# Kernel tuning notes

Measured on AMD Instinct MI355X. Metric: run time of the kernel, lower is better.

The kernel has to match this reference:

```python
import jax, jax.numpy as jnp
import numpy as np

L, B, D = 2048, 8, 2048


def setup_inputs() -> dict:
    key = jax.random.key(0)
    k1, k2, k3 = jax.random.split(key, 3)
    x = jax.random.normal(k1, (L, B, D), dtype=jnp.float32)
    x_mix_last = jnp.zeros((B, D), dtype=jnp.float32)
    factor_param = jax.random.uniform(k2, (D,), dtype=jnp.float32)
    W = jax.random.normal(k3, (D, D), dtype=jnp.float32) * (1.0 / np.sqrt(D))
    return {"x": x, "x_mix_last": x_mix_last, "factor_param": factor_param, "W": W}


def reference(x, x_mix_last, factor_param, W):
    seq_len = x.shape[0]
    factor = jax.nn.sigmoid(factor_param)                      # [D]
    t = jnp.arange(seq_len, dtype=x.dtype)[:, None]            # [L,1]
    factor_progression = jnp.power(factor[None, :], t)         # [L,D] = factor**t
    # FFT-based causal convolution: y[t] = sum_{s<=t} factor**(t-s) * x[s]
    n = 2 * seq_len
    fft_fp = jnp.fft.rfft(factor_progression, n=n, axis=0)     # [L+1, D]
    fft_x = jnp.fft.rfft(x, n=n, axis=0)                       # [L+1, B, D]
    conv = jnp.fft.irfft(fft_x * fft_fp[:, None, :], axis=0)[:seq_len]  # [L,B,D]
    conv = conv.astype(x.dtype)
    # EMA mix: carried state decays as factor**(t+1); new input weighted by (1-factor)
    x_mix = (x_mix_last[None, :, :] * factor_progression[:, None, :] * factor
             + (1.0 - factor) * conv)                          # [L,B,D]
    # Linear mixing W (no bias): out = x_mix @ W.T
    return jnp.einsum('lbd,ed->lbe', x_mix, W)
```

## Files before the change

kernel.cpp:

```cpp
#include <hip/hip_runtime.h>
#include <hip/hip_bf16.h>
#include <stdint.h>

#define L_SEQ 2048
#define BATCH 8
#define DIM   2048
#define M_DIM (L_SEQ * BATCH)
#define N_DIM DIM
#define K_DIM DIM

typedef short bf16x8 __attribute__((ext_vector_type(8)));
typedef float f32x4  __attribute__((ext_vector_type(4)));
typedef unsigned short u16x4 __attribute__((ext_vector_type(4)));

__device__ inline unsigned short f2bf_rn(float f) {
    unsigned int u = __float_as_uint(f);
    u += 0x7FFF + ((u >> 16) & 1);
    return (unsigned short)(u >> 16);
}

__device__ inline void gload16(const void* g, void* l) {
    __builtin_amdgcn_global_load_lds(
        (const __attribute__((address_space(1))) void*)g,
        (__attribute__((address_space(3))) void*)l, 16, 0, 0);
}

__global__ void cvt_w_kernel(const float* __restrict__ W,
                             unsigned short* __restrict__ Wb) {
    int i = blockIdx.x * 256 + threadIdx.x;
    const float4 v = *reinterpret_cast<const float4*>(W + (size_t)i * 4);
    u16x4 r;
    r.x = f2bf_rn(v.x); r.y = f2bf_rn(v.y);
    r.z = f2bf_rn(v.z); r.w = f2bf_rn(v.w);
    *reinterpret_cast<u16x4*>(Wb + (size_t)i * 4) = r;
}

#define SCAN_CHUNK 256
#define SCAN_LB    128
__global__ void ema_scan_kernel(const float* __restrict__ x,
                                const float* __restrict__ xml,
                                const float* __restrict__ fparam,
                                unsigned short* __restrict__ xm) {
    int g  = blockIdx.x * 256 + threadIdx.x;
    int d  = g & (DIM - 1);
    int b  = (g >> 11) & (BATCH - 1);
    int ch = g >> 14;

    const float p  = fparam[d];
    const float f  = 1.0f / (1.0f + expf(-p));
    const float xl = xml[b * DIM + d];
    const float omf = 1.0f - f;

    const int t0 = ch * SCAN_CHUNK;
    int tstart = t0 - SCAN_LB; if (tstart < 0) tstart = 0;
    const int stride = BATCH * DIM;

    const float* xp = x + (size_t)tstart * stride + b * DIM + d;
    float conv = 0.0f;
    #pragma unroll 4
    for (int t = tstart; t < t0; ++t) {
        conv = fmaf(conv, f, *xp);
        xp += stride;
    }
    float pw = powf(f, (float)(t0 + 1));
    unsigned short* op = xm + (size_t)t0 * stride + b * DIM + d;
    #pragma unroll 4
    for (int t = 0; t < SCAN_CHUNK; ++t) {
        conv = fmaf(conv, f, *xp);
        float r = fmaf(xl, pw, omf * conv);
        *op = f2bf_rn(r);
        pw *= f;
        xp += stride; op += stride;
    }
}

#define BM 128
#define BN 128
#define BK 32

__global__ void gemm_bt_kernel(const unsigned short* __restrict__ A,
                               const unsigned short* __restrict__ Bt,
                               float* __restrict__ C) {
    __shared__ unsigned short lds_a[2][BM * BK];
    __shared__ unsigned short lds_b[2][BN * BK];

    int bid = blockIdx.x;
    int swz = (bid & 7) * 256 + (bid >> 3);
    int tm = swz >> 4;
    int tn = swz & 15;

    const int tid  = threadIdx.x;
    const int lane = tid & 63;
    const int w    = tid >> 6;
    const int wm   = (w >> 1) * 64;
    const int wn   = (w & 1) * 64;

    const int c0 = tid, c1 = tid + 256;
    const char* gA = (const char*)(A  + (size_t)tm * BM * K_DIM);
    const char* gB = (const char*)(Bt + (size_t)tn * BN * K_DIM);
    const char* pa0 = gA + (size_t)(c0 >> 2) * (K_DIM * 2) + (c0 & 3) * 16;
    const char* pa1 = gA + (size_t)(c1 >> 2) * (K_DIM * 2) + (c1 & 3) * 16;
    const char* pb0 = gB + (size_t)(c0 >> 2) * (K_DIM * 2) + (c0 & 3) * 16;
    const char* pb1 = gB + (size_t)(c1 >> 2) * (K_DIM * 2) + (c1 & 3) * 16;

#define STAGE(buf, t) do {                                   \
        size_t ko = (size_t)(t) * (BK * 2);                  \
        gload16(pa0 + ko, &lds_a[buf][c0 * 8]);              \
        gload16(pa1 + ko, &lds_a[buf][c1 * 8]);              \
        gload16(pb0 + ko, &lds_b[buf][c0 * 8]);              \
        gload16(pb1 + ko, &lds_b[buf][c1 * 8]);              \
    } while (0)

    f32x4 acc[4][4];
    #pragma unroll
    for (int m = 0; m < 4; ++m)
        #pragma unroll
        for (int n = 0; n < 4; ++n)
            acc[m][n] = (f32x4){0.f, 0.f, 0.f, 0.f};

    STAGE(0, 0);
    __syncthreads();

    const int rsel = lane & 15;
    const int kb   = (lane >> 4) * 8;

    int cur = 0;
    const int NT = K_DIM / BK;
    for (int t = 0; t < NT; ++t) {
        if (t + 1 < NT) STAGE(cur ^ 1, t + 1);

        bf16x8 afr[4], bfr[4];
        #pragma unroll
        for (int m = 0; m < 4; ++m)
            afr[m] = *(const bf16x8*)&lds_a[cur][(wm + m * 16 + rsel) * BK + kb];
        #pragma unroll
        for (int n = 0; n < 4; ++n)
            bfr[n] = *(const bf16x8*)&lds_b[cur][(wn + n * 16 + rsel) * BK + kb];

        #pragma unroll
        for (int m = 0; m < 4; ++m)
            #pragma unroll
            for (int n = 0; n < 4; ++n)
                acc[m][n] = __builtin_amdgcn_mfma_f32_16x16x32_bf16(
                    afr[m], bfr[n], acc[m][n], 0, 0, 0);

        __syncthreads();
        cur ^= 1;
    }

    float* Cp = C + (size_t)(tm * BM + wm) * N_DIM + tn * BN + wn;
    const int col = lane & 15;
    const int rg  = (lane >> 4) * 4;
    #pragma unroll
    for (int m = 0; m < 4; ++m)
        #pragma unroll
        for (int n = 0; n < 4; ++n)
            #pragma unroll
            for (int j = 0; j < 4; ++j)
                Cp[(size_t)(m * 16 + rg + j) * N_DIM + n * 16 + col] = acc[m][n][j];
#undef STAGE
}

extern "C" void kernel_launch(void* const* d_in, const int* in_sizes, int n_in,
                              void* d_out, int out_size, void* d_ws, size_t ws_size,
                              hipStream_t stream) {
    const float* x   = (const float*)d_in[0];
    const float* xml = (const float*)d_in[1];
    const float* fp  = (const float*)d_in[2];
    const float* W   = (const float*)d_in[3];
    float* out = (float*)d_out;

    unsigned short* xmix = (unsigned short*)d_ws;
    unsigned short* wb   = xmix + (size_t)M_DIM * K_DIM;

    cvt_w_kernel<<<4096, 256, 0, stream>>>(W, wb);
    ema_scan_kernel<<<512, 256, 0, stream>>>(x, xml, fp, xmix);
    gemm_bt_kernel<<<(M_DIM / BM) * (N_DIM / BN), 256, 0, stream>>>(xmix, wb, out);
}
```

Before: 449.3 us.

## Replace GEMM with 256x256 swizzled-LDS pipelined kernel and vectorize EMA scan

Replaces the 128x128 bf16 GEMM with a 256x256 tile, 512-thread kernel using 64-wide K tiles, XOR-swizzled LDS, and an eight-phase interleaved prefetch/MFMA schedule with explicit waitcnt and priority hints. The aim is higher operand reuse and better overlap of global loads with matrix math. The EMA scan now processes two channels per thread with float2 loads and uses shorter chunks and lookback for more parallelism. The GEMM uses 128KB of dynamic LDS, which limits occupancy, and the hand-tuned wait counts must match the load order exactly.

```diff
diff --git a/kernel.cpp b/kernel.cpp
--- a/kernel.cpp
+++ b/kernel.cpp
@@ -35,130 +35,180 @@
     *reinterpret_cast<u16x4*>(Wb + (size_t)i * 4) = r;
 }
 
-#define SCAN_CHUNK 256
-#define SCAN_LB    128
+#define SCH 128
+#define SLB 64
 __global__ void ema_scan_kernel(const float* __restrict__ x,
                                 const float* __restrict__ xml,
                                 const float* __restrict__ fparam,
                                 unsigned short* __restrict__ xm) {
     int g  = blockIdx.x * 256 + threadIdx.x;
-    int d  = g & (DIM - 1);
-    int b  = (g >> 11) & (BATCH - 1);
-    int ch = g >> 14;
-
-    const float p  = fparam[d];
-    const float f  = 1.0f / (1.0f + expf(-p));
-    const float xl = xml[b * DIM + d];
-    const float omf = 1.0f - f;
-
-    const int t0 = ch * SCAN_CHUNK;
-    int tstart = t0 - SCAN_LB; if (tstart < 0) tstart = 0;
-    const int stride = BATCH * DIM;
-
-    const float* xp = x + (size_t)tstart * stride + b * DIM + d;
-    float conv = 0.0f;
-    #pragma unroll 4
-    for (int t = tstart; t < t0; ++t) {
-        conv = fmaf(conv, f, *xp);
-        xp += stride;
+    int dp = (g & 1023) * 2;
+    int b  = (g >> 10) & (BATCH - 1);
+    int ch = g >> 13;
+
+    float2 pv = *reinterpret_cast<const float2*>(fparam + dp);
+    const float f0 = 1.0f / (1.0f + expf(-pv.x));
+    const float f1 = 1.0f / (1.0f + expf(-pv.y));
+    float2 xlv = *reinterpret_cast<const float2*>(xml + b * DIM + dp);
+    const float om0 = 1.0f - f0, om1 = 1.0f - f1;
+
+    const int t0 = ch * SCH;
+    int ts = t0 - SLB; if (ts < 0) ts = 0;
+    const int stride2 = (BATCH * DIM) / 2;
+
+    const float2* xp = reinterpret_cast<const float2*>(x) +
+                       (size_t)ts * stride2 + (b * DIM + dp) / 2;
+    float c0 = 0.0f, c1 = 0.0f;
+    #pragma unroll 8
+    for (int t = ts; t < t0; ++t) {
+        float2 v = *xp;
+        c0 = fmaf(c0, f0, v.x);
+        c1 = fmaf(c1, f1, v.y);
+        xp += stride2;
     }
-    float pw = powf(f, (float)(t0 + 1));
-    unsigned short* op = xm + (size_t)t0 * stride + b * DIM + d;
-    #pragma unroll 4
-    for (int t = 0; t < SCAN_CHUNK; ++t) {
-        conv = fmaf(conv, f, *xp);
-        float r = fmaf(xl, pw, omf * conv);
-        *op = f2bf_rn(r);
-        pw *= f;
-        xp += stride; op += stride;
+    float pw0 = powf(f0, (float)(t0 + 1));
+    float pw1 = powf(f1, (float)(t0 + 1));
+    ushort2* op = reinterpret_cast<ushort2*>(xm + (size_t)t0 * BATCH * DIM + b * DIM + dp);
+    #pragma unroll 8
+    for (int k = 0; k < SCH; ++k) {
+        float2 v = *xp;
+        c0 = fmaf(c0, f0, v.x);
+        c1 = fmaf(c1, f1, v.y);
+        ushort2 r;
+        r.x = f2bf_rn(fmaf(xlv.x, pw0, om0 * c0));
+        r.y = f2bf_rn(fmaf(xlv.y, pw1, om1 * c1));
+        *op = r;
+        pw0 *= f0; pw1 *= f1;
+        xp += stride2; op += stride2;
     }
 }
 
-#define BM 128
-#define BN 128
-#define BK 32
-
-__global__ void gemm_bt_kernel(const unsigned short* __restrict__ A,
-                               const unsigned short* __restrict__ Bt,
-                               float* __restrict__ C) {
-    __shared__ unsigned short lds_a[2][BM * BK];
-    __shared__ unsigned short lds_b[2][BN * BK];
+#define NT_K (K_DIM / 64)
+#define NI   (NT_K / 2)
+
+__global__ void __launch_bounds__(512, 2)
+gemm8_kernel(const unsigned short* __restrict__ A,
+             const unsigned short* __restrict__ Bt,
+             float* __restrict__ C) {
+    extern __shared__ __attribute__((aligned(16))) char smem[];
 
     int bid = blockIdx.x;
-    int swz = (bid & 7) * 256 + (bid >> 3);
-    int tm = swz >> 4;
-    int tn = swz & 15;
+    int swz = (bid & 7) * 64 + (bid >> 3);
+    const int tm = swz >> 3;
+    const int tn = swz & 7;
 
     const int tid  = threadIdx.x;
     const int lane = tid & 63;
     const int w    = tid >> 6;
-    const int wm   = (w >> 1) * 64;
-    const int wn   = (w & 1) * 64;
-
-    const int c0 = tid, c1 = tid + 256;
-    const char* gA = (const char*)(A  + (size_t)tm * BM * K_DIM);
-    const char* gB = (const char*)(Bt + (size_t)tn * BN * K_DIM);
-    const char* pa0 = gA + (size_t)(c0 >> 2) * (K_DIM * 2) + (c0 & 3) * 16;
-    const char* pa1 = gA + (size_t)(c1 >> 2) * (K_DIM * 2) + (c1 & 3) * 16;
-    const char* pb0 = gB + (size_t)(c0 >> 2) * (K_DIM * 2) + (c0 & 3) * 16;
-    const char* pb1 = gB + (size_t)(c1 >> 2) * (K_DIM * 2) + (c1 & 3) * 16;
-
-#define STAGE(buf, t) do {                                   \
-        size_t ko = (size_t)(t) * (BK * 2);                  \
-        gload16(pa0 + ko, &lds_a[buf][c0 * 8]);              \
-        gload16(pa1 + ko, &lds_a[buf][c1 * 8]);              \
-        gload16(pb0 + ko, &lds_b[buf][c0 * 8]);              \
-        gload16(pb1 + ko, &lds_b[buf][c1 * 8]);              \
+    const int wr   = w >> 2;
+    const int wn   = w & 3;
+
+    const int aoff0 = (tid >> 3) * (K_DIM * 2) + (((tid & 7) ^ ((tid >> 3) & 7)) * 16);
+    const int aoff1 = aoff0 + 64 * (K_DIM * 2);
+    const char* gAc = (const char*)(A  + (size_t)tm * 256 * K_DIM);
+    const char* gBc = (const char*)(Bt + (size_t)tn * 256 * K_DIM);
+
+#define STAGE_A(bs, ha, t) do {                                              \
+        const char* _s = gAc + (size_t)((ha) * 128) * (K_DIM * 2) + (size_t)(t) * 128; \
+        char* _d = smem + (bs) * 65536 + (ha) * 16384 + tid * 16;            \
+        gload16(_s + aoff0, _d);                                             \
+        gload16(_s + aoff1, _d + 8192);                                      \
     } while (0)
-
-    f32x4 acc[4][4];
+#define STAGE_B(bs, hb, t) do {                                              \
+        const char* _s = gBc + (size_t)((hb) * 128) * (K_DIM * 2) + (size_t)(t) * 128; \
+        char* _d = smem + (bs) * 65536 + 32768 + (hb) * 16384 + tid * 16;    \
+        gload16(_s + aoff0, _d);                                             \
+        gload16(_s + aoff1, _d + 8192);                                      \
+    } while (0)
+
+    const int ra   = wr * 64 + (lane & 15);
+    const int rb   = wn * 32 + (lane & 15);
+    const int khi  = (lane >> 4) * 16;
+    const int cxor = (lane & 7) << 4;
+
+    f32x4 acc[8][4];
     #pragma unroll
-    for (int m = 0; m < 4; ++m)
+    for (int m = 0; m < 8; ++m)
         #pragma unroll
         for (int n = 0; n < 4; ++n)
             acc[m][n] = (f32x4){0.f, 0.f, 0.f, 0.f};
 
-    STAGE(0, 0);
-    __syncthreads();
-
-    const int rsel = lane & 15;
-    const int kb   = (lane >> 4) * 8;
-
-    int cur = 0;
-    const int NT = K_DIM / BK;
-    for (int t = 0; t < NT; ++t) {
-        if (t + 1 < NT) STAGE(cur ^ 1, t + 1);
-
-        bf16x8 afr[4], bfr[4];
-        #pragma unroll
-        for (int m = 0; m < 4; ++m)
-            afr[m] = *(const bf16x8*)&lds_a[cur][(wm + m * 16 + rsel) * BK + kb];
-        #pragma unroll
-        for (int n = 0; n < 4; ++n)
-            bfr[n] = *(const bf16x8*)&lds_b[cur][(wn + n * 16 + rsel) * BK + kb];
-
+#define PHASE(qa, qb, bs, VN, ...) do {                                      \
+        const char* _ab = smem + (bs) * 65536;                               \
+        const char* _bb = _ab + 32768;                                       \
+        bf16x8 afr[4][2], bfr[2][2];                                         \
+        _Pragma("unroll") for (int m = 0; m < 4; ++m) {                      \
+            int _r = (qa) * 128 + ra + m * 16;                               \
+            _Pragma("unroll") for (int ks = 0; ks < 2; ++ks)                 \
+                afr[m][ks] = *(const bf16x8*)(_ab + _r * 128 +               \
+                                              ((ks * 64 + khi) ^ cxor));     \
+        }                                                                    \
+        _Pragma("unroll") for (int n = 0; n < 2; ++n) {                      \
+            int _rn = (qb) * 128 + rb + n * 16;                              \
+            _Pragma("unroll") for (int ks = 0; ks < 2; ++ks)                 \
+                bfr[n][ks] = *(const bf16x8*)(_bb + _rn * 128 +              \
+                                              ((ks * 64 + khi) ^ cxor));     \
+        }                                                                    \
+        __VA_ARGS__;                                                         \
+        __builtin_amdgcn_s_barrier();                                        \
+        __builtin_amdgcn_s_setprio(1);                                       \
+        _Pragma("unroll") for (int m = 0; m < 4; ++m)                        \
+            _Pragma("unroll") for (int n = 0; n < 2; ++n)                    \
+                _Pragma("unroll") for (int ks = 0; ks < 2; ++ks)             \
+                    acc[(qa) * 4 + m][(qb) * 2 + n] =                        \
+                        __builtin_amdgcn_mfma_f32_16x16x32_bf16(             \
+                            afr[m][ks], bfr[n][ks],                          \
+                            acc[(qa) * 4 + m][(qb) * 2 + n], 0, 0, 0);       \
+        __builtin_amdgcn_s_setprio(0);                                       \
+        asm volatile("s_waitcnt vmcnt(" #VN ")" ::: "memory");               \
+        __builtin_amdgcn_s_barrier();                                        \
+    } while (0)
+
+    STAGE_A(0, 0, 0); STAGE_B(0, 0, 0); STAGE_B(0, 1, 0); STAGE_A(0, 1, 0);
+    asm volatile("s_waitcnt vmcnt(4)" ::: "memory");
+    __builtin_amdgcn_s_barrier();
+
+    for (int i = 0; i < NI - 1; ++i) {
+        const int t1 = 2 * i + 1, t2 = 2 * i + 2;
+        PHASE(0, 0, 0, 4, STAGE_A(1, 0, t1));
+        PHASE(0, 1, 0, 4, STAGE_B(1, 0, t1));
+        PHASE(1, 0, 0, 4, STAGE_B(1, 1, t1));
+        PHASE(1, 1, 0, 4, STAGE_A(1, 1, t1));
+        PHASE(0, 0, 1, 4, STAGE_A(0, 0, t2));
+        PHASE(0, 1, 1, 4, STAGE_B(0, 0, t2));
+        PHASE(1, 0, 1, 4, STAGE_B(0, 1, t2));
+        PHASE(1, 1, 1, 4, STAGE_A(0, 1, t2));
+    }
+    PHASE(0, 0, 0, 4, STAGE_A(1, 0, NT_K - 1));
+    PHASE(0, 1, 0, 4, STAGE_B(1, 0, NT_K - 1));
+    PHASE(1, 0, 0, 4, STAGE_B(1, 1, NT_K - 1));
+    PHASE(1, 1, 0, 4, STAGE_A(1, 1, NT_K - 1));
+    PHASE(0, 0, 1, 2, (void)0);
+    PHASE(0, 1, 1, 0, (void)0);
+    PHASE(1, 0, 1, 0, (void)0);
+    PHASE(1, 1, 1, 0, (void)0);
+
+    float* Cb = C + (size_t)(tm * 256) * N_DIM + tn * 256;
+    const int col0 = lane & 15;
+    const int rg   = (lane >> 4) * 4;
+    #pragma unroll
+    for (int qa2 = 0; qa2 < 2; ++qa2)
         #pragma unroll
         for (int m = 0; m < 4; ++m)
             #pragma unroll
-            for (int n = 0; n < 4; ++n)
-                acc[m][n] = __builtin_amdgcn_mfma_f32_16x16x32_bf16(
-                    afr[m], bfr[n], acc[m][n], 0, 0, 0);
-
-        __syncthreads();
-        cur ^= 1;
-    }
-
-    float* Cp = C + (size_t)(tm * BM + wm) * N_DIM + tn * BN + wn;
-    const int col = lane & 15;
-    const int rg  = (lane >> 4) * 4;
-    #pragma unroll
-    for (int m = 0; m < 4; ++m)
-        #pragma unroll
-        for (int n = 0; n < 4; ++n)
-            #pragma unroll
-            for (int j = 0; j < 4; ++j)
-                Cp[(size_t)(m * 16 + rg + j) * N_DIM + n * 16 + col] = acc[m][n][j];
-#undef STAGE
+            for (int j = 0; j < 4; ++j) {
+                int row = qa2 * 128 + wr * 64 + m * 16 + rg + j;
+                float* rp = Cb + (size_t)row * N_DIM;
+                #pragma unroll
+                for (int qb2 = 0; qb2 < 2; ++qb2)
+                    #pragma unroll
+                    for (int n = 0; n < 2; ++n)
+                        rp[qb2 * 128 + wn * 32 + n * 16 + col0] =
+                            acc[qa2 * 4 + m][qb2 * 2 + n][j];
+            }
+#undef PHASE
+#undef STAGE_A
+#undef STAGE_B
 }
 
 extern "C" void kernel_launch(void* const* d_in, const int* in_sizes, int n_in,
@@ -173,7 +223,10 @@
     unsigned short* xmix = (unsigned short*)d_ws;
     unsigned short* wb   = xmix + (size_t)M_DIM * K_DIM;
 
+    (void)hipFuncSetAttribute(reinterpret_cast<const void*>(&gemm8_kernel),
+                              hipFuncAttributeMaxDynamicSharedMemorySize, 131072);
+
     cvt_w_kernel<<<4096, 256, 0, stream>>>(W, wb);
     ema_scan_kernel<<<512, 256, 0, stream>>>(x, xml, fp, xmix);
-    gemm_bt_kernel<<<(M_DIM / BM) * (N_DIM / BN), 256, 0, stream>>>(xmix, wb, out);
-}
+    gemm8_kernel<<<(M_DIM / 256) * (N_DIM / 256), 512, 131072, stream>>>(xmix, wb, out);
+}
```

After: 378.6 us. 1.19x faster.
